# Kernel tuning notes

Measured on AMD Instinct MI355X. Metric: run time of the kernel, lower is better.

The kernel has to match this reference:

```python
import jax, jax.numpy as jnp
import numpy as np

B = 8192
FULL_DIM = 4096
HEADS = 16
MLP_DIM = 16384
CHUNKS = 4
HEAD_IN = FULL_DIM // HEADS      # 256
HEAD_OUT = MLP_DIM // HEADS      # 1024
CHUNK = HEAD_IN // CHUNKS        # 64


def _chunk_random_perm(rng):
    # PermuteIn(mode='chunk_random'): permute 64-wide chunks across full_dim
    n_chunks = FULL_DIM // CHUNK
    chunk_idx = rng.permutation(n_chunks)
    perm = np.concatenate([np.arange(CHUNK) + i * CHUNK for i in chunk_idx])
    return perm.astype(np.int32)


def setup_inputs() -> dict:
    key = jax.random.key(0)
    k1, k2, k3 = jax.random.split(key, 3)
    rng = np.random.default_rng(0)
    # xavier_uniform with relu gain = sqrt(2) on (in_dim, out_dim) matrices
    gain = np.sqrt(2.0)
    bound_up = gain * np.sqrt(6.0 / (HEAD_IN + HEAD_OUT))
    bound_dn = gain * np.sqrt(6.0 / (HEAD_OUT + HEAD_IN))
    return {
        "x": jax.random.normal(k1, (B, FULL_DIM), dtype=jnp.float32),
        "perm": jnp.asarray(_chunk_random_perm(rng)),
        "w_up": jax.random.uniform(k2, (HEADS, HEAD_IN, HEAD_OUT), jnp.float32, -bound_up, bound_up),
        "b_up": jnp.zeros((MLP_DIM,), jnp.float32),
        "w_down": jax.random.uniform(k3, (HEADS, HEAD_OUT, HEAD_IN), jnp.float32, -bound_dn, bound_dn),
        "b_down": jnp.zeros((FULL_DIM,), jnp.float32),
    }


def reference(x, perm, w_up, b_up, w_down, b_down):
    b = x.shape[0]
    unperm = jnp.argsort(perm)  # inverse permutation (Unpermute)
    # PermuteIn
    h = x[:, perm]
    # up: per-head grouped GEMM + bias
    h = h.reshape(b, HEADS, HEAD_IN)
    h = jnp.einsum('bhd,hdl->bhl', h, w_up).reshape(b, MLP_DIM) + b_up
    # GELU (exact, matching torch nn.GELU default)
    h = jax.nn.gelu(h, approximate=False)
    # down: per-head grouped GEMM + bias
    h = h.reshape(b, HEADS, HEAD_OUT)
    h = jnp.einsum('bhd,hdl->bhl', h, w_down).reshape(b, FULL_DIM) + b_down
    # Unpermute
    return h[:, unperm]
```

## Files before the change

### kernel.cpp

```cpp
#include <hip/hip_runtime.h>
#include <hip/hip_bf16.h>
#include <math.h>

#define HEADS    16
#define HEAD_IN  256
#define HEAD_OUT 1024
#define FULLD    4096
#define BM       128
#define NC       32
#define NCHUNKS  (HEAD_OUT / NC)
#define THREADS  512
#define LDK      264
#define LDK2     40
#define LDO      264

typedef short  short8 __attribute__((ext_vector_type(8)));
typedef float  f32x4  __attribute__((ext_vector_type(4)));

__device__ __forceinline__ ushort f2bf(float f) {
    union { float f; unsigned u; } x; x.f = f;
    unsigned r = x.u + 0x7fffu + ((x.u >> 16) & 1u);
    return (ushort)(r >> 16);
}

__device__ __forceinline__ float fast_gelu(float v) {
    float v2 = v * v;
    float p  = __builtin_fmaf(v2, 0.044715f, 1.0f);
    float a  = v * p * -2.3021254f;
    float e  = __builtin_amdgcn_exp2f(a);
    float r  = __builtin_amdgcn_rcpf(1.0f + e);
    return v * r;
}

__global__ void __launch_bounds__(256) transpose_head(const float* __restrict__ in,
                                                      ushort* __restrict__ out,
                                                      int R, int C) {
    __shared__ __align__(16) ushort tile[64][68];
    int h = blockIdx.z;
    const float* ip = in  + (size_t)h * R * C;
    ushort*      op = out + (size_t)h * R * C;
    int t  = threadIdx.x;
    int cr = t & 15;
    int rr = t >> 4;
    int r0 = blockIdx.x * 64, c0 = blockIdx.y * 64;
    #pragma unroll
    for (int p = 0; p < 4; ++p) {
        int r = rr + p * 16;
        float4 v = *(const float4*)&ip[(size_t)(r0 + r) * C + c0 + cr * 4];
        tile[r][cr*4+0] = f2bf(v.x); tile[r][cr*4+1] = f2bf(v.y);
        tile[r][cr*4+2] = f2bf(v.z); tile[r][cr*4+3] = f2bf(v.w);
    }
    __syncthreads();
    #pragma unroll
    for (int p = 0; p < 4; ++p) {
        int c = rr + p * 16;
        ushort4 v;
        v.x = tile[cr*4+0][c]; v.y = tile[cr*4+1][c];
        v.z = tile[cr*4+2][c]; v.w = tile[cr*4+3][c];
        *(ushort4*)&op[(size_t)(c0 + c) * R + r0 + cr * 4] = v;
    }
}

__global__ void __launch_bounds__(THREADS, 2)
fused_mlp(const float* __restrict__ x, const int* __restrict__ perm,
          const ushort* __restrict__ wupT, const float* __restrict__ bup,
          const ushort* __restrict__ wdnT, const float* __restrict__ bdn,
          float* __restrict__ out) {
    __shared__ __align__(16) ushort smem[NC*LDK + HEAD_IN*LDK2 + BM*LDK2];
    ushort* sW1 = smem;
    ushort* sW2 = smem + NC*LDK;
    ushort* sT  = sW2 + HEAD_IN*LDK2;

    const int t    = threadIdx.x;
    const int wave = t >> 6;
    const int lane = t & 63;
    const int q    = lane >> 4;
    const int r    = lane & 15;
    const int h    = blockIdx.y;
    const int m0   = blockIdx.x * BM;

    short8 xf[8];
    {
        const size_t rowoff = (size_t)(m0 + wave*16 + r) * FULLD;
        #pragma unroll
        for (int ks = 0; ks < 8; ++ks) {
            int c0 = ks*32 + q*8;
            int g  = perm[h*HEAD_IN + c0];
            const float* p = x + rowoff + g;
            float4 a = *(const float4*)p;
            float4 b = *(const float4*)(p + 4);
            short8 v;
            v[0] = (short)f2bf(a.x); v[1] = (short)f2bf(a.y);
            v[2] = (short)f2bf(a.z); v[3] = (short)f2bf(a.w);
            v[4] = (short)f2bf(b.x); v[5] = (short)f2bf(b.y);
            v[6] = (short)f2bf(b.z); v[7] = (short)f2bf(b.w);
            xf[ks] = v;
        }
    }

    const int i10 = t, i11 = THREADS + t;
    const ushort* g1a = wupT + (((size_t)h*HEAD_OUT + (i10>>5)) << 8) + (i10&31)*8;
    const ushort* g1b = wupT + (((size_t)h*HEAD_OUT + (i11>>5)) << 8) + (i11&31)*8;
    const ushort* g2a = wdnT + (((size_t)h*HEAD_IN  + (i10>>2)) << 10) + (i10&3)*8;
    const ushort* g2b = wdnT + (((size_t)h*HEAD_IN  + (i11>>2)) << 10) + (i11&3)*8;
    ushort* l1a = sW1 + (i10>>5)*LDK + (i10&31)*8;
    ushort* l1b = sW1 + (i11>>5)*LDK + (i11&31)*8;
    ushort* l2a = sW2 + (i10>>2)*LDK2 + (i10&3)*8;
    ushort* l2b = sW2 + (i11>>2)*LDK2 + (i11&3)*8;

    short8 w1ra = *(const short8*)g1a;
    short8 w1rb = *(const short8*)g1b;
    short8 w2ra = *(const short8*)g2a;
    short8 w2rb = *(const short8*)g2b;

    f32x4 oacc[16];
    #pragma unroll
    for (int i = 0; i < 16; ++i) oacc[i] = (f32x4){0.f, 0.f, 0.f, 0.f};

    for (int ch = 0; ch < NCHUNKS; ++ch) {
        const int n0 = ch * NC;
        __syncthreads();
        *(short8*)l1a = w1ra;  *(short8*)l1b = w1rb;
        *(short8*)l2a = w2ra;  *(short8*)l2b = w2rb;
        __syncthreads();

        if (ch + 1 < NCHUNKS) {
            const size_t d1 = (size_t)(ch + 1) * NC * 256;
            const size_t d2 = (size_t)(ch + 1) * NC;
            w1ra = *(const short8*)(g1a + d1);
            w1rb = *(const short8*)(g1b + d1);
            w2ra = *(const short8*)(g2a + d2);
            w2rb = *(const short8*)(g2b + d2);
        }

        f32x4 tacc[2];
        #pragma unroll
        for (int i = 0; i < 2; ++i) tacc[i] = (f32x4){0.f, 0.f, 0.f, 0.f};
        #pragma unroll
        for (int ks = 0; ks < 8; ++ks) {
            const int ko = ks*32 + q*8;
            #pragma unroll
            for (int nf = 0; nf < 2; ++nf) {
                short8 bfr = *(const short8*)(sW1 + (nf*16 + r)*LDK + ko);
                tacc[nf] = __builtin_amdgcn_mfma_f32_16x16x32_bf16(xf[ks], bfr, tacc[nf], 0, 0, 0);
            }
        }
        #pragma unroll
        for (int nf = 0; nf < 2; ++nf) {
            float bias = bup[h*HEAD_OUT + n0 + nf*16 + r];
            #pragma unroll
            for (int rg = 0; rg < 4; ++rg) {
                float v = tacc[nf][rg] + bias;
                sT[(wave*16 + q*4 + rg)*LDK2 + nf*16 + r] = f2bf(fast_gelu(v));
            }
        }
        {
            short8 af = *(const short8*)(sT + (wave*16 + r)*LDK2 + q*8);
            #pragma unroll
            for (int nf2 = 0; nf2 < 16; ++nf2) {
                short8 bfr = *(const short8*)(sW2 + (nf2*16 + r)*LDK2 + q*8);
                oacc[nf2] = __builtin_amdgcn_mfma_f32_16x16x32_bf16(af, bfr, oacc[nf2], 0, 0, 0);
            }
        }
    }

    float* sOutF = (float*)smem;
    #pragma unroll
    for (int quar = 0; quar < 4; ++quar) {
        __syncthreads();
        if ((wave >> 1) == quar) {
            int wl = wave & 1;
            #pragma unroll
            for (int nf2 = 0; nf2 < 16; ++nf2) {
                float bias = bdn[h*HEAD_IN + nf2*16 + r];
                #pragma unroll
                for (int rg = 0; rg < 4; ++rg) {
                    sOutF[(wl*16 + q*4 + rg)*LDO + nf2*16 + r] = oacc[nf2][rg] + bias;
                }
            }
        }
        __syncthreads();
        #pragma unroll
        for (int i = 0; i < 2; ++i) {
            int idx  = i*THREADS + t;
            int mr   = idx >> 5;
            int sg   = idx & 31;
            int ccol = sg * 8;
            int g    = perm[h*HEAD_IN + ccol];
            float4 v0 = *(const float4*)(sOutF + mr*LDO + ccol);
            float4 v1 = *(const float4*)(sOutF + mr*LDO + ccol + 4);
            float* dst = out + (size_t)(m0 + quar*32 + mr)*FULLD + g;
            *(float4*)dst       = v0;
            *(float4*)(dst + 4) = v1;
        }
    }
}

extern "C" void kernel_launch(void* const* d_in, const int* in_sizes, int n_in,
                              void* d_out, int out_size, void* d_ws, size_t ws_size,
                              hipStream_t stream) {
    const float* x    = (const float*)d_in[0];
    const int*   perm = (const int*)d_in[1];
    const float* wup  = (const float*)d_in[2];
    const float* bup  = (const float*)d_in[3];
    const float* wdn  = (const float*)d_in[4];
    const float* bdn  = (const float*)d_in[5];
    float* out = (float*)d_out;

    const int Bt = in_sizes[0] / FULLD;
    const size_t wcount = (size_t)HEADS * HEAD_IN * HEAD_OUT;

    ushort* wupT = (ushort*)d_ws;
    ushort* wdnT = wupT + wcount;

    transpose_head<<<dim3(HEAD_IN/64,  HEAD_OUT/64, HEADS), 256, 0, stream>>>(wup, wupT, HEAD_IN,  HEAD_OUT);
    transpose_head<<<dim3(HEAD_OUT/64, HEAD_IN/64,  HEADS), 256, 0, stream>>>(wdn, wdnT, HEAD_OUT, HEAD_IN);

    dim3 grid(Bt / BM, HEADS, 1);
    fused_mlp<<<grid, THREADS, 0, stream>>>(x, perm, wupT, bup, wdnT, bdn, out);
}
```

Before: 538.3 us.

## Switch fused MLP to 32x32x16 MFMA with async LDS double buffering

```diff
diff --git a/kernel.cpp b/kernel.cpp
--- a/kernel.cpp
+++ b/kernel.cpp
@@ -9,13 +9,20 @@
 #define BM       128
 #define NC       32
 #define NCHUNKS  (HEAD_OUT / NC)
-#define THREADS  512
-#define LDK      264
-#define LDK2     40
-#define LDO      264
+#define THREADS  256
+#define LDO      268
 
 typedef short  short8 __attribute__((ext_vector_type(8)));
 typedef float  f32x4  __attribute__((ext_vector_type(4)));
+typedef float  f32x16 __attribute__((ext_vector_type(16)));
+typedef unsigned int u32;
+
+#define AS_GLOBAL __attribute__((address_space(1)))
+#define AS_LOCAL  __attribute__((address_space(3)))
+
+__device__ __forceinline__ void gload_lds16(const void* g, void* l) {
+    __builtin_amdgcn_global_load_lds((const AS_GLOBAL u32*)g, (AS_LOCAL u32*)l, 16, 0, 0);
+}
 
 __device__ __forceinline__ ushort f2bf(float f) {
     union { float f; unsigned u; } x; x.f = f;
@@ -66,129 +73,144 @@
           const ushort* __restrict__ wupT, const float* __restrict__ bup,
           const ushort* __restrict__ wdnT, const float* __restrict__ bdn,
           float* __restrict__ out) {
-    __shared__ __align__(16) ushort smem[NC*LDK + HEAD_IN*LDK2 + BM*LDK2];
-    ushort* sW1 = smem;
-    ushort* sW2 = smem + NC*LDK;
-    ushort* sT  = sW2 + HEAD_IN*LDK2;
+    __shared__ __align__(16) char smem[2 * 32768];
 
     const int t    = threadIdx.x;
     const int wave = t >> 6;
     const int lane = t & 63;
-    const int q    = lane >> 4;
-    const int r    = lane & 15;
+    const int rho  = lane & 31;
+    const int h5   = lane >> 5;
     const int h    = blockIdx.y;
     const int m0   = blockIdx.x * BM;
 
-    short8 xf[8];
+    const ushort* g1b[4];
+    const ushort* g2b[4];
+    #pragma unroll
+    for (int p = 0; p < 4; ++p) {
+        int row = p*8 + wave*2 + h5;
+        int n   = (row & 0x13) | ((row & 4) << 1) | ((row & 8) >> 1);
+        g1b[p] = wupT + (((size_t)h*HEAD_OUT + n) << 8) + (rho ^ (row & 7)) * 8;
+        int d  = p*64 + wave*16 + (lane >> 2);
+        g2b[p] = wdnT + (((size_t)h*HEAD_IN + d) << 10) + ((lane & 3) ^ (d & 3)) * 8;
+    }
+    char* l1b = smem + wave*1024;
+    char* l2b = smem + 16384 + wave*1024;
+
+    #pragma unroll
+    for (int p = 0; p < 4; ++p) {
+        gload_lds16(g1b[p], l1b + p*4096);
+        gload_lds16(g2b[p], l2b + p*4096);
+    }
+
+    short8 xf[16];
     {
-        const size_t rowoff = (size_t)(m0 + wave*16 + r) * FULLD;
-        #pragma unroll
-        for (int ks = 0; ks < 8; ++ks) {
-            int c0 = ks*32 + q*8;
-            int g  = perm[h*HEAD_IN + c0];
-            const float* p = x + rowoff + g;
-            float4 a = *(const float4*)p;
-            float4 b = *(const float4*)(p + 4);
+        const float* xrow = x + (size_t)(m0 + wave*32 + rho) * FULLD;
+        #pragma unroll
+        for (int ks = 0; ks < 16; ++ks) {
+            int g = perm[h*HEAD_IN + ks*16 + h5*8];
+            float4 a = *(const float4*)(xrow + g);
+            float4 b = *(const float4*)(xrow + g + 4);
             short8 v;
-            v[0] = (short)f2bf(a.x); v[1] = (short)f2bf(a.y);
-            v[2] = (short)f2bf(a.z); v[3] = (short)f2bf(a.w);
-            v[4] = (short)f2bf(b.x); v[5] = (short)f2bf(b.y);
-            v[6] = (short)f2bf(b.z); v[7] = (short)f2bf(b.w);
+            v[0]=(short)f2bf(a.x); v[1]=(short)f2bf(a.y);
+            v[2]=(short)f2bf(a.z); v[3]=(short)f2bf(a.w);
+            v[4]=(short)f2bf(b.x); v[5]=(short)f2bf(b.y);
+            v[6]=(short)f2bf(b.z); v[7]=(short)f2bf(b.w);
             xf[ks] = v;
         }
     }
 
-    const int i10 = t, i11 = THREADS + t;
-    const ushort* g1a = wupT + (((size_t)h*HEAD_OUT + (i10>>5)) << 8) + (i10&31)*8;
-    const ushort* g1b = wupT + (((size_t)h*HEAD_OUT + (i11>>5)) << 8) + (i11&31)*8;
-    const ushort* g2a = wdnT + (((size_t)h*HEAD_IN  + (i10>>2)) << 10) + (i10&3)*8;
-    const ushort* g2b = wdnT + (((size_t)h*HEAD_IN  + (i11>>2)) << 10) + (i11&3)*8;
-    ushort* l1a = sW1 + (i10>>5)*LDK + (i10&31)*8;
-    ushort* l1b = sW1 + (i11>>5)*LDK + (i11&31)*8;
-    ushort* l2a = sW2 + (i10>>2)*LDK2 + (i10&3)*8;
-    ushort* l2b = sW2 + (i11>>2)*LDK2 + (i11&3)*8;
-
-    short8 w1ra = *(const short8*)g1a;
-    short8 w1rb = *(const short8*)g1b;
-    short8 w2ra = *(const short8*)g2a;
-    short8 w2rb = *(const short8*)g2b;
-
-    f32x4 oacc[16];
-    #pragma unroll
-    for (int i = 0; i < 16; ++i) oacc[i] = (f32x4){0.f, 0.f, 0.f, 0.f};
+    f32x16 oacc[8];
+    #pragma unroll
+    for (int i = 0; i < 8; ++i)
+        #pragma unroll
+        for (int e = 0; e < 16; ++e) oacc[i][e] = 0.f;
+
+    const float* bupb = bup + h*HEAD_OUT + h5*8;
+    const int x1 = rho & 7;
+    const int x2 = rho & 3;
+
+    __syncthreads();
 
     for (int ch = 0; ch < NCHUNKS; ++ch) {
-        const int n0 = ch * NC;
+        const int buf = (ch & 1) * 32768;
+
+        if (ch + 1 < NCHUNKS) {
+            const int nbuf = ((ch + 1) & 1) * 32768;
+            const size_t d1 = (size_t)(ch + 1) * (NC * 256);
+            const size_t d2 = (size_t)(ch + 1) * NC;
+            #pragma unroll
+            for (int p = 0; p < 4; ++p) {
+                gload_lds16(g1b[p] + d1, l1b + nbuf + p*4096);
+                gload_lds16(g2b[p] + d2, l2b + nbuf + p*4096);
+            }
+        }
+
+        const char* s1 = smem + buf + rho*512;
+        f32x16 te, to;
+        #pragma unroll
+        for (int e = 0; e < 16; ++e) { te[e] = 0.f; to[e] = 0.f; }
+        #pragma unroll
+        for (int ks = 0; ks < 16; ks += 2) {
+            short8 w0 = *(const short8*)(s1 + ((((ks    )*2 + h5) ^ x1) * 16));
+            short8 w1 = *(const short8*)(s1 + ((((ks + 1)*2 + h5) ^ x1) * 16));
+            te = __builtin_amdgcn_mfma_f32_32x32x16_bf16(w0, xf[ks],     te, 0, 0, 0);
+            to = __builtin_amdgcn_mfma_f32_32x32x16_bf16(w1, xf[ks + 1], to, 0, 0, 0);
+        }
+
+        short8 a2[2];
+        #pragma unroll
+        for (int kk = 0; kk < 2; ++kk) {
+            f32x4 bA = *(const f32x4*)(bupb + ch*NC + kk*16);
+            f32x4 bB = *(const f32x4*)(bupb + ch*NC + kk*16 + 4);
+            short8 v;
+            #pragma unroll
+            for (int e = 0; e < 4; ++e) {
+                float u0 = te[kk*8 + e]     + to[kk*8 + e]     + bA[e];
+                float u1 = te[kk*8 + 4 + e] + to[kk*8 + 4 + e] + bB[e];
+                v[e]     = (short)f2bf(fast_gelu(u0));
+                v[4 + e] = (short)f2bf(fast_gelu(u1));
+            }
+            a2[kk] = v;
+        }
+
+        const char* s2 = smem + buf + 16384 + rho*64;
+        #pragma unroll
+        for (int kk = 0; kk < 2; ++kk) {
+            #pragma unroll
+            for (int dt = 0; dt < 8; ++dt) {
+                short8 b = *(const short8*)(s2 + dt*2048 + (((kk*2 + h5) ^ x2) * 16));
+                oacc[dt] = __builtin_amdgcn_mfma_f32_32x32x16_bf16(a2[kk], b, oacc[dt], 0, 0, 0);
+            }
+        }
+
         __syncthreads();
-        *(short8*)l1a = w1ra;  *(short8*)l1b = w1rb;
-        *(short8*)l2a = w2ra;  *(short8*)l2b = w2rb;
-        __syncthreads();
-
-        if (ch + 1 < NCHUNKS) {
-            const size_t d1 = (size_t)(ch + 1) * NC * 256;
-            const size_t d2 = (size_t)(ch + 1) * NC;
-            w1ra = *(const short8*)(g1a + d1);
-            w1rb = *(const short8*)(g1b + d1);
-            w2ra = *(const short8*)(g2a + d2);
-            w2rb = *(const short8*)(g2b + d2);
-        }
-
-        f32x4 tacc[2];
-        #pragma unroll
-        for (int i = 0; i < 2; ++i) tacc[i] = (f32x4){0.f, 0.f, 0.f, 0.f};
-        #pragma unroll
-        for (int ks = 0; ks < 8; ++ks) {
-            const int ko = ks*32 + q*8;
-            #pragma unroll
-            for (int nf = 0; nf < 2; ++nf) {
-                short8 bfr = *(const short8*)(sW1 + (nf*16 + r)*LDK + ko);
-                tacc[nf] = __builtin_amdgcn_mfma_f32_16x16x32_bf16(xf[ks], bfr, tacc[nf], 0, 0, 0);
-            }
-        }
-        #pragma unroll
-        for (int nf = 0; nf < 2; ++nf) {
-            float bias = bup[h*HEAD_OUT + n0 + nf*16 + r];
-            #pragma unroll
-            for (int rg = 0; rg < 4; ++rg) {
-                float v = tacc[nf][rg] + bias;
-                sT[(wave*16 + q*4 + rg)*LDK2 + nf*16 + r] = f2bf(fast_gelu(v));
-            }
-        }
-        {
-            short8 af = *(const short8*)(sT + (wave*16 + r)*LDK2 + q*8);
-            #pragma unroll
-            for (int nf2 = 0; nf2 < 16; ++nf2) {
-                short8 bfr = *(const short8*)(sW2 + (nf2*16 + r)*LDK2 + q*8);
-                oacc[nf2] = __builtin_amdgcn_mfma_f32_16x16x32_bf16(af, bfr, oacc[nf2], 0, 0, 0);
-            }
-        }
     }
 
     float* sOutF = (float*)smem;
     #pragma unroll
     for (int quar = 0; quar < 4; ++quar) {
         __syncthreads();
-        if ((wave >> 1) == quar) {
-            int wl = wave & 1;
-            #pragma unroll
-            for (int nf2 = 0; nf2 < 16; ++nf2) {
-                float bias = bdn[h*HEAD_IN + nf2*16 + r];
+        if (wave == quar) {
+            #pragma unroll
+            for (int dt = 0; dt < 8; ++dt) {
+                const float bias = bdn[h*HEAD_IN + dt*32 + rho];
                 #pragma unroll
-                for (int rg = 0; rg < 4; ++rg) {
-                    sOutF[(wl*16 + q*4 + rg)*LDO + nf2*16 + r] = oacc[nf2][rg] + bias;
+                for (int rg = 0; rg < 16; ++rg) {
+                    int row = (rg & 3) + 8*(rg >> 2) + 4*h5;
+                    sOutF[row*LDO + dt*32 + rho] = oacc[dt][rg] + bias;
                 }
             }
         }
         __syncthreads();
         #pragma unroll
-        for (int i = 0; i < 2; ++i) {
-            int idx  = i*THREADS + t;
-            int mr   = idx >> 5;
-            int sg   = idx & 31;
-            int ccol = sg * 8;
-            int g    = perm[h*HEAD_IN + ccol];
-            float4 v0 = *(const float4*)(sOutF + mr*LDO + ccol);
-            float4 v1 = *(const float4*)(sOutF + mr*LDO + ccol + 4);
+        for (int i = 0; i < 4; ++i) {
+            int idx = i*THREADS + t;
+            int mr  = idx >> 5;
+            int sg  = idx & 31;
+            int g   = perm[h*HEAD_IN + sg*8];
+            const float* src = sOutF + mr*LDO + sg*8;
+            float4 v0 = *(const float4*)src;
+            float4 v1 = *(const float4*)(src + 4);
             float* dst = out + (size_t)(m0 + quar*32 + mr)*FULLD + g;
             *(float4*)dst       = v0;
             *(float4*)(dst + 4) = v1;
```

New measurement: 478.2 us. -11.2%, faster.
